# Kernel optimization log

Hardware: AMD Instinct MI355X
Metric: run time of the kernel (lower is better)

## Reference

```python
import jax, jax.numpy as jnp
import numpy as np

B, L, E, H = 512, 100, 256, 256
T = 100          # max_length (== sourceL for TSP)
C_EXPLORE = 10.0  # tanh_exploration
N_GLIMPSES = 1


def setup_inputs() -> dict:
    key = jax.random.key(0)
    ks = jax.random.split(key, 19)
    s = 0.05
    f = lambda k, shape: jax.random.normal(k, shape, dtype=jnp.float32) * s
    return dict(
        decoder_input=f(ks[0], (B, E)),
        embedded_inputs=f(ks[1], (L, B, E)),
        h0=f(ks[2], (B, H)), c0=f(ks[3], (B, H)),
        context=f(ks[4], (L, B, H)),
        Wi=f(ks[5], (4 * H, E)), bi=f(ks[6], (4 * H,)),
        Wh=f(ks[7], (4 * H, H)), bh=f(ks[8], (4 * H,)),
        g_Wq=f(ks[9], (H, H)), g_bq=f(ks[10], (H,)),
        g_Wref=f(ks[11], (H, H)), g_bref=f(ks[12], (H,)),
        g_v=f(ks[13], (H,)),
        p_Wq=f(ks[14], (H, H)), p_bq=f(ks[15], (H,)),
        p_Wref=f(ks[16], (H, H)), p_bref=f(ks[17], (H,)),
        p_v=f(ks[18], (H,)),
    )


def _decode(decoder_input, embedded_inputs, h0, c0, context,
            Wi, bi, Wh, bh,
            g_Wq, g_bq, g_Wref, g_bref, g_v,
            p_Wq, p_bq, p_Wref, p_bref, p_v):
    # Conv1d(dim, dim, 1) over context == feature matmul; context is static,
    # so project refs once (same math as per-step projection in torch code).
    ctx = jnp.transpose(context, (1, 2, 0))                       # [B,H,L]
    e_g = jnp.einsum('oh,bhl->bol', g_Wref, ctx) + g_bref[None, :, None]
    e_p = jnp.einsum('oh,bhl->bol', p_Wref, ctx) + p_bref[None, :, None]
    rows = jnp.arange(B)

    def attn_logits(q, e, Wq, bq, v):
        qp = q @ Wq.T + bq                                        # [B,H]
        return jnp.einsum('h,bhl->bl', v, jnp.tanh(qp[:, :, None] + e))

    def apply_mask(step, logits, mask, prev):
        # step 0: mask position 0; step 1: unmask 0, mask prev; step>1: mask prev
        m1 = jnp.where(step == 1, mask.at[:, 0].set(False), mask)
        m1 = m1.at[rows, prev].set(True)
        m0 = mask.at[:, 0].set(True)
        new_mask = jnp.where(step == 0, m0, m1)
        return jnp.where(new_mask, -jnp.inf, logits), new_mask

    def step_fn(carry, step):
        x, hx, cx, mask, prev = carry
        gates = x @ Wi.T + bi + hx @ Wh.T + bh                    # [B,4H]
        ig, fg, cg, og = jnp.split(gates, 4, axis=1)
        cy = jax.nn.sigmoid(fg) * cx + jax.nn.sigmoid(ig) * jnp.tanh(cg)
        hy = jax.nn.sigmoid(og) * jnp.tanh(cy)
        g_l = hy
        for _ in range(N_GLIMPSES):
            lg = attn_logits(g_l, e_g, g_Wq, g_bq, g_v)
            lg, mask = apply_mask(step, lg, mask, prev)
            g_l = jnp.einsum('bhl,bl->bh', e_g, jax.nn.softmax(lg, axis=1))
        lp = attn_logits(g_l, e_p, p_Wq, p_bq, p_v)
        lp = C_EXPLORE * jnp.tanh(lp)                             # use_tanh=True
        lp, mask = apply_mask(step, lp, mask, prev)
        probs = jax.nn.softmax(lp, axis=1)                        # [B,L]
        idxs = jnp.argmax(probs, axis=1)                          # greedy
        sels = embedded_inputs[idxs, rows, :]                     # [B,E]
        return (sels, hy, cy, mask, idxs), (probs, idxs)

    mask0 = jnp.zeros((B, L), dtype=bool)
    prev0 = jnp.zeros((B,), dtype=jnp.int32)
    carry0 = (decoder_input, h0, c0, mask0, prev0)
    (xT, hx, cx, maskT, prevT), (probs_seq, sel_seq) = jax.lax.scan(
        step_fn, carry0, jnp.arange(T))
    return probs_seq, sel_seq, hx, cx


def reference(decoder_input, embedded_inputs, h0, c0, context,
              Wi, bi, Wh, bh,
              g_Wq, g_bq, g_Wref, g_bref, g_v,
              p_Wq, p_bq, p_Wref, p_bref, p_v):
    return _decode(decoder_input, embedded_inputs, h0, c0, context,
                   Wi, bi, Wh, bh,
                   g_Wq, g_bq, g_Wref, g_bref, g_v,
                   p_Wq, p_bq, p_Wref, p_bref, p_v)
```

## Files before the change

kernel.cpp:

```cpp
#include <hip/hip_runtime.h>
#include <math.h>

namespace {

constexpr int Bn = 512;
constexpr int Ln = 100;
constexpr int En = 256;
constexpr int Hn = 256;
constexpr int Tn = 100;

__device__ __forceinline__ float fast_tanh(float x) {
  float ax = fabsf(x);
  float e = __expf(-2.0f * ax);
  float t = (1.0f - e) / (1.0f + e);
  return copysignf(t, x);
}
__device__ __forceinline__ float fast_sigm(float x) {
  return 1.0f / (1.0f + __expf(-x));
}

__device__ __forceinline__ float wave_max(float v) {
#pragma unroll
  for (int off = 32; off > 0; off >>= 1) v = fmaxf(v, __shfl_xor(v, off, 64));
  return v;
}
__device__ __forceinline__ float wave_sum(float v) {
#pragma unroll
  for (int off = 32; off > 0; off >>= 1) v += __shfl_xor(v, off, 64);
  return v;
}

__global__ void init_kernel(const float* __restrict__ dec, const float* __restrict__ h0,
                            const float* __restrict__ c0, float* __restrict__ x,
                            float* __restrict__ h, float* __restrict__ c,
                            int* __restrict__ mask, int* __restrict__ prev) {
  int i = blockIdx.x * 256 + threadIdx.x;
  if (i < Bn * En) x[i] = dec[i];
  if (i < Bn * Hn) { h[i] = h0[i]; c[i] = c0[i]; }
  if (i < Bn * Ln) mask[i] = 0;
  if (i < Bn) prev[i] = 0;
}

__global__ void transpose256_kernel(const float* __restrict__ W, float* __restrict__ WT) {
  int h = blockIdx.x, k = threadIdx.x;
  WT[k * 256 + h] = W[h * 256 + k];
}

__global__ void matmul_M_kernel(const float* __restrict__ pWq,
                                const float* __restrict__ gWref,
                                float* __restrict__ M) {
  int i = blockIdx.x, j = threadIdx.x;
  float acc = 0.0f;
  for (int h = 0; h < 256; ++h) acc += pWq[i * 256 + h] * gWref[h * 256 + j];
  M[i * 256 + j] = acc;
}

__global__ void mb_kernel(const float* __restrict__ pWq,
                          const float* __restrict__ gbref,
                          float* __restrict__ mb) {
  __shared__ float gb[256];
  int i = threadIdx.x;
  gb[i] = gbref[i];
  __syncthreads();
  float acc = 0.0f;
  for (int h = 0; h < 256; ++h) acc += pWq[i * 256 + h] * gb[h];
  mb[i] = acc;
}

__global__ __launch_bounds__(256) void precompute_e_kernel(
    const float* __restrict__ WT, const float* __restrict__ bref,
    const float* __restrict__ context, float* __restrict__ e_t) {
  int b = blockIdx.x;
  int l0 = blockIdx.y * 25;
  int h = threadIdx.x;
  __shared__ float ctx_s[25][256];
  for (int li = 0; li < 25; ++li)
    ctx_s[li][h] = context[((size_t)(l0 + li) * Bn + b) * Hn + h];
  __syncthreads();
  float acc[25];
  float bias = bref[h];
#pragma unroll
  for (int li = 0; li < 25; ++li) acc[li] = bias;
  for (int k = 0; k < 256; ++k) {
    float w = WT[k * 256 + h];
#pragma unroll
    for (int li = 0; li < 25; ++li) acc[li] += w * ctx_s[li][k];
  }
#pragma unroll
  for (int li = 0; li < 25; ++li)
    e_t[((size_t)b * Ln + (l0 + li)) * Hn + h] = acc[li];
}

__global__ __launch_bounds__(256) void lstm_kernel(
    const float* __restrict__ x, const float* __restrict__ h_in,
    const float* __restrict__ c_in, const float* __restrict__ Wi,
    const float* __restrict__ Wh, const float* __restrict__ bi,
    const float* __restrict__ bh, float* __restrict__ h_out,
    float* __restrict__ c_out) {
  const int b0 = blockIdx.x * 32;
  const int n0 = blockIdx.y * 16;
  const int tid = threadIdx.x;
  const int n = tid & 15;
  const int br = tid >> 4;
  __shared__ float A_s[32][33];
  __shared__ float W_s[4][16][33];
  float acc[4][2];
  const int nn = n0 + n;
#pragma unroll
  for (int g = 0; g < 4; ++g) {
    float bias = bi[g * 256 + nn] + bh[g * 256 + nn];
    acc[g][0] = bias;
    acc[g][1] = bias;
  }
  const int bb = tid >> 3, q = tid & 7;
  for (int k0 = 0; k0 < 512; k0 += 32) {
    const float* Asrc = (k0 < 256) ? x : h_in;
    const float* Wsrc = (k0 < 256) ? Wi : Wh;
    const int kb = k0 & 255;
    __syncthreads();
    float4 av = *(const float4*)(Asrc + (b0 + bb) * 256 + kb + q * 4);
    A_s[q * 4 + 0][bb] = av.x;
    A_s[q * 4 + 1][bb] = av.y;
    A_s[q * 4 + 2][bb] = av.z;
    A_s[q * 4 + 3][bb] = av.w;
#pragma unroll
    for (int s = 0; s < 2; ++s) {
      int sl = tid + s * 256;
      int g = sl >> 7;
      int nl = (sl >> 3) & 15;
      int qq = sl & 7;
      float4 wv = *(const float4*)(Wsrc + ((g * 256 + n0 + nl) * 256) + kb + qq * 4);
      W_s[g][nl][qq * 4 + 0] = wv.x;
      W_s[g][nl][qq * 4 + 1] = wv.y;
      W_s[g][nl][qq * 4 + 2] = wv.z;
      W_s[g][nl][qq * 4 + 3] = wv.w;
    }
    __syncthreads();
#pragma unroll
    for (int kk = 0; kk < 32; ++kk) {
      float a0 = A_s[kk][2 * br];
      float a1 = A_s[kk][2 * br + 1];
#pragma unroll
      for (int g = 0; g < 4; ++g) {
        float w = W_s[g][n][kk];
        acc[g][0] += a0 * w;
        acc[g][1] += a1 * w;
      }
    }
  }
#pragma unroll
  for (int m = 0; m < 2; ++m) {
    int b = b0 + 2 * br + m;
    float ig = acc[0][m], fg = acc[1][m], cg = acc[2][m], og = acc[3][m];
    float cold = c_in[b * 256 + nn];
    float cy = fast_sigm(fg) * cold + fast_sigm(ig) * fast_tanh(cg);
    float hy = fast_sigm(og) * fast_tanh(cy);
    c_out[b * 256 + nn] = cy;
    h_out[b * 256 + nn] = hy;
  }
}

__global__ __launch_bounds__(256) void qp_gemm_kernel(
    const float* __restrict__ A, const float* __restrict__ Wq,
    const float* __restrict__ bq, float* __restrict__ C) {
  const int b0 = blockIdx.x * 32;
  const int n0 = blockIdx.y * 16;
  const int tid = threadIdx.x;
  const int n = tid & 15;
  const int br = tid >> 4;
  __shared__ float A_s[32][33];
  __shared__ float W_s[16][33];
  float bias = bq[n0 + n];
  float acc0 = bias, acc1 = bias;
  const int bb = tid >> 3, q = tid & 7;
  for (int k0 = 0; k0 < 256; k0 += 32) {
    __syncthreads();
    float4 av = *(const float4*)(A + (b0 + bb) * 256 + k0 + q * 4);
    A_s[q * 4 + 0][bb] = av.x;
    A_s[q * 4 + 1][bb] = av.y;
    A_s[q * 4 + 2][bb] = av.z;
    A_s[q * 4 + 3][bb] = av.w;
    if (tid < 128) {
      int nl = tid >> 3, qq = tid & 7;
      float4 wv = *(const float4*)(Wq + (n0 + nl) * 256 + k0 + qq * 4);
      W_s[nl][qq * 4 + 0] = wv.x;
      W_s[nl][qq * 4 + 1] = wv.y;
      W_s[nl][qq * 4 + 2] = wv.z;
      W_s[nl][qq * 4 + 3] = wv.w;
    }
    __syncthreads();
#pragma unroll
    for (int kk = 0; kk < 32; ++kk) {
      float a0 = A_s[kk][2 * br];
      float a1 = A_s[kk][2 * br + 1];
      float w = W_s[n][kk];
      acc0 += a0 * w;
      acc1 += a1 * w;
    }
  }
  C[(b0 + 2 * br) * 256 + n0 + n] = acc0;
  C[(b0 + 2 * br + 1) * 256 + n0 + n] = acc1;
}

__global__ __launch_bounds__(256) void attn_fused_kernel(
    const float* __restrict__ qp_g, const float* __restrict__ gv,
    const float* __restrict__ pv, const float* __restrict__ pbq,
    const float* __restrict__ e_g, const float* __restrict__ f_p,
    const float* __restrict__ e_p, int* __restrict__ mask,
    int* __restrict__ prev, const float* __restrict__ emb,
    float* __restrict__ xout, float* __restrict__ out, int step) {
  const int tid = threadIdx.x;
  const int b = blockIdx.x;
  const int li = tid & 127;
  const int half = tid >> 7;
  __shared__ float q1_s[256], vg_s[256], vp_s[256], q2_s[256];
  __shared__ float logit_s[128], p_s[128];
  __shared__ float wred_m[2], wred_s[2];
  __shared__ float wval[2];
  __shared__ int widx[2];
  __shared__ int sel_s;
  q1_s[tid] = qp_g[b * 256 + tid];
  vg_s[tid] = gv[tid];
  vp_s[tid] = pv[tid];
  __syncthreads();
  float part = 0.0f;
  if (li < Ln) {
    const float4* ep = (const float4*)(e_g + ((size_t)b * Ln + li) * Hn + half * 128);
    const float4* q4 = (const float4*)(q1_s + half * 128);
    const float4* v4 = (const float4*)(vg_s + half * 128);
#pragma unroll 8
    for (int j = 0; j < 32; ++j) {
      float4 ev = ep[j];
      float4 qv = q4[j];
      float4 vv = v4[j];
      part += vv.x * fast_tanh(qv.x + ev.x);
      part += vv.y * fast_tanh(qv.y + ev.y);
      part += vv.z * fast_tanh(qv.z + ev.z);
      part += vv.w * fast_tanh(qv.w + ev.w);
    }
  }
  if (half == 1) logit_s[li] = part;
  __syncthreads();
  float lgv = -INFINITY;
  int mreg = 1;
  if (half == 0 && li < Ln) {
    float a = part + logit_s[li];
    int pb = prev[b];
    int m = mask[b * Ln + li];
    if (step == 0) {
      if (li == 0) m = 1;
    } else {
      if (step == 1 && li == 0) m = 0;
      if (li == pb) m = 1;
    }
    mask[b * Ln + li] = m;
    mreg = m;
    lgv = m ? -INFINITY : a;
  }
  float wm = wave_max((tid < 128) ? lgv : -INFINITY);
  if (tid < 128 && (tid & 63) == 0) wred_m[tid >> 6] = wm;
  __syncthreads();
  float mx = fmaxf(wred_m[0], wred_m[1]);
  float pvv = (lgv == -INFINITY) ? 0.0f : __expf(lgv - mx);
  float wsm = wave_sum((tid < 128) ? pvv : 0.0f);
  if (tid < 128 && (tid & 63) == 0) wred_s[tid >> 6] = wsm;
  __syncthreads();
  float tot = wred_s[0] + wred_s[1];
  if (tid < 128) p_s[li] = pvv / tot;
  __syncthreads();
  {
    float acc = pbq[tid];
    const float* fb = f_p + (size_t)b * Ln * Hn + tid;
#pragma unroll 4
    for (int l = 0; l < Ln; ++l) acc += p_s[l] * fb[(size_t)l * Hn];
    q2_s[tid] = acc;
  }
  __syncthreads();
  part = 0.0f;
  if (li < Ln) {
    const float4* ep = (const float4*)(e_p + ((size_t)b * Ln + li) * Hn + half * 128);
    const float4* q4 = (const float4*)(q2_s + half * 128);
    const float4* v4 = (const float4*)(vp_s + half * 128);
#pragma unroll 8
    for (int j = 0; j < 32; ++j) {
      float4 ev = ep[j];
      float4 qv = q4[j];
      float4 vv = v4[j];
      part += vv.x * fast_tanh(qv.x + ev.x);
      part += vv.y * fast_tanh(qv.y + ev.y);
      part += vv.z * fast_tanh(qv.z + ev.z);
      part += vv.w * fast_tanh(qv.w + ev.w);
    }
  }
  if (half == 1) logit_s[li] = part;
  __syncthreads();
  lgv = -INFINITY;
  if (half == 0 && li < Ln) {
    float a = part + logit_s[li];
    float lp = 10.0f * fast_tanh(a);
    lgv = mreg ? -INFINITY : lp;
  }
  wm = wave_max((tid < 128) ? lgv : -INFINITY);
  if (tid < 128 && (tid & 63) == 0) wred_m[tid >> 6] = wm;
  __syncthreads();
  mx = fmaxf(wred_m[0], wred_m[1]);
  pvv = (lgv == -INFINITY) ? 0.0f : __expf(lgv - mx);
  wsm = wave_sum((tid < 128) ? pvv : 0.0f);
  if (tid < 128 && (tid & 63) == 0) wred_s[tid >> 6] = wsm;
  __syncthreads();
  tot = wred_s[0] + wred_s[1];
  float p = pvv / tot;
  if (half == 0 && li < Ln) out[((size_t)step * Bn + b) * Ln + li] = p;
  float val = (tid < 128 && li < Ln) ? p : -1.0f;
  int idx = li;
#pragma unroll
  for (int off = 32; off > 0; off >>= 1) {
    float ov = __shfl_down(val, off, 64);
    int oi = __shfl_down(idx, off, 64);
    if (ov > val || (ov == val && oi < idx)) { val = ov; idx = oi; }
  }
  if (tid < 128 && (tid & 63) == 0) { wval[tid >> 6] = val; widx[tid >> 6] = idx; }
  __syncthreads();
  if (tid == 0) {
    int sel = (wval[1] > wval[0] || (wval[1] == wval[0] && widx[1] < widx[0]))
                  ? widx[1] : widx[0];
    sel_s = sel;
    prev[b] = sel;
    out[(size_t)Tn * Bn * Ln + (size_t)step * Bn + b] = (float)sel;
  }
  __syncthreads();
  int sel = sel_s;
  xout[b * En + tid] = emb[((size_t)sel * Bn + b) * En + tid];
}

__global__ void finalize_kernel(const float* __restrict__ h,
                                const float* __restrict__ c,
                                float* __restrict__ out) {
  int i = blockIdx.x * 256 + threadIdx.x;
  const size_t base = (size_t)Tn * Bn * Ln + (size_t)Tn * Bn;
  if (i < Bn * Hn) {
    out[base + i] = h[i];
    out[base + (size_t)Bn * Hn + i] = c[i];
  }
}

}

extern "C" void kernel_launch(void* const* d_in, const int* in_sizes, int n_in,
                              void* d_out, int out_size, void* d_ws, size_t ws_size,
                              hipStream_t stream) {
  (void)in_sizes; (void)n_in; (void)out_size; (void)ws_size;
  const float* dec   = (const float*)d_in[0];
  const float* emb   = (const float*)d_in[1];
  const float* h0    = (const float*)d_in[2];
  const float* c0    = (const float*)d_in[3];
  const float* ctx   = (const float*)d_in[4];
  const float* Wi    = (const float*)d_in[5];
  const float* bi    = (const float*)d_in[6];
  const float* Wh    = (const float*)d_in[7];
  const float* bh    = (const float*)d_in[8];
  const float* gWq   = (const float*)d_in[9];
  const float* gbq   = (const float*)d_in[10];
  const float* gWref = (const float*)d_in[11];
  const float* gbref = (const float*)d_in[12];
  const float* gv    = (const float*)d_in[13];
  const float* pWq   = (const float*)d_in[14];
  const float* pbq   = (const float*)d_in[15];
  const float* pWref = (const float*)d_in[16];
  const float* pbref = (const float*)d_in[17];
  const float* pv    = (const float*)d_in[18];

  float* ws = (float*)d_ws;
  float* e_g   = ws;  ws += (size_t)Bn * Hn * Ln;
  float* e_p   = ws;  ws += (size_t)Bn * Hn * Ln;
  float* f_p   = ws;  ws += (size_t)Bn * Hn * Ln;
  float* WTg   = ws;  ws += 256 * 256;
  float* WTp   = ws;  ws += 256 * 256;
  float* Mbuf  = ws;  ws += 256 * 256;
  float* MT    = ws;  ws += 256 * 256;
  float* mb    = ws;  ws += 256;
  float* xbuf  = ws;  ws += Bn * En;
  float* hbuf  = ws;  ws += 2 * Bn * Hn;
  float* cbuf  = ws;  ws += 2 * Bn * Hn;
  float* qpg   = ws;  ws += Bn * Hn;
  int* maskb   = (int*)ws;  ws += Bn * Ln;
  int* prevb   = (int*)ws;  ws += Bn;
  float* out = (float*)d_out;

  init_kernel<<<512, 256, 0, stream>>>(dec, h0, c0, xbuf, hbuf, cbuf, maskb, prevb);
  transpose256_kernel<<<256, 256, 0, stream>>>(gWref, WTg);
  transpose256_kernel<<<256, 256, 0, stream>>>(pWref, WTp);
  matmul_M_kernel<<<256, 256, 0, stream>>>(pWq, gWref, Mbuf);
  mb_kernel<<<1, 256, 0, stream>>>(pWq, gbref, mb);
  transpose256_kernel<<<256, 256, 0, stream>>>(Mbuf, MT);
  precompute_e_kernel<<<dim3(512, 4), 256, 0, stream>>>(WTg, gbref, ctx, e_g);
  precompute_e_kernel<<<dim3(512, 4), 256, 0, stream>>>(WTp, pbref, ctx, e_p);
  precompute_e_kernel<<<dim3(512, 4), 256, 0, stream>>>(MT, mb, ctx, f_p);

  for (int t = 0; t < Tn; ++t) {
    const float* hin = hbuf + (t & 1) * Bn * Hn;
    float* hout      = hbuf + ((t + 1) & 1) * Bn * Hn;
    const float* cin = cbuf + (t & 1) * Bn * Hn;
    float* cout      = cbuf + ((t + 1) & 1) * Bn * Hn;
    lstm_kernel<<<dim3(16, 16), 256, 0, stream>>>(xbuf, hin, cin, Wi, Wh, bi, bh, hout, cout);
    qp_gemm_kernel<<<dim3(16, 16), 256, 0, stream>>>(hout, gWq, gbq, qpg);
    attn_fused_kernel<<<512, 256, 0, stream>>>(qpg, gv, pv, pbq, e_g, f_p, e_p,
                                               maskb, prevb, emb, xbuf, out, t);
  }
  finalize_kernel<<<512, 256, 0, stream>>>(hbuf, cbuf, out);
}
```

Before: 8.001 ms.

## Fuse the per-step decode loop into a single persistent cooperative kernel

Replaces the 300 per-step kernel launches (LSTM GEMM, query GEMM, attention) with one cooperative persistent kernel. It uses grid.sync between the gate GEMM phase and the per-batch attention phase, and computes the glimpse query projection inside each block from a transposed Wq. The goal is to remove launch overhead and intermediate global round-trips. In exchange it adds two grid-wide barriers per step and fixes the grid at 256 blocks, which limits parallelism in the attention phase. It falls back to the old multi-kernel path if the cooperative launch fails.

```diff
diff --git a/kernel.cpp b/kernel.cpp
--- a/kernel.cpp
+++ b/kernel.cpp
@@ -1,5 +1,8 @@
 #include <hip/hip_runtime.h>
+#include <hip/hip_cooperative_groups.h>
 #include <math.h>
+
+namespace cg = cooperative_groups;
 
 namespace {
 
@@ -89,6 +92,248 @@
 #pragma unroll
   for (int li = 0; li < 25; ++li)
     e_t[((size_t)b * Ln + (l0 + li)) * Hn + h] = acc[li];
+}
+
+__global__ __launch_bounds__(256) void persistent_kernel(
+    const float* __restrict__ Wi, const float* __restrict__ Wh,
+    const float* __restrict__ bi, const float* __restrict__ bh,
+    const float* __restrict__ WqTg, const float* __restrict__ gbq,
+    const float* __restrict__ gv, const float* __restrict__ pv,
+    const float* __restrict__ pbq, const float* __restrict__ e_g,
+    const float* __restrict__ f_p, const float* __restrict__ e_p,
+    float* __restrict__ gates, float* __restrict__ xbuf,
+    float* __restrict__ hbuf, float* __restrict__ cbuf,
+    int* __restrict__ mask, int* __restrict__ prev,
+    const float* __restrict__ emb, float* __restrict__ out) {
+  cg::grid_group grid = cg::this_grid();
+  const int blk = blockIdx.x;
+  const int tid = threadIdx.x;
+
+  __shared__ union SM {
+    struct { float A[64][36]; float W[32][36]; } l;
+    struct {
+      float hs[256], q1[256], q2[256], vg[256], vp[256];
+      float qtmp[4][256];
+      float logit[128], p[128];
+      float wred_m[2], wred_s[2], wval[2];
+      int widx[2];
+      int sel;
+    } a;
+  } sm;
+
+  const int nt = blk & 31;
+  const int bt = blk >> 5;
+  const int n0 = nt * 32;
+  const int b0 = bt * 64;
+  const int tx = tid & 15;
+  const int ty = tid >> 4;
+  const int li = tid & 127;
+  const int half = tid >> 7;
+  const size_t hbase = (size_t)Tn * Bn * Ln + (size_t)Tn * Bn;
+  const size_t cbase = hbase + (size_t)Bn * Hn;
+
+  for (int t = 0; t < Tn; ++t) {
+    float acc[4][2];
+    {
+      float bias0 = bi[n0 + 2 * ty] + bh[n0 + 2 * ty];
+      float bias1 = bi[n0 + 2 * ty + 1] + bh[n0 + 2 * ty + 1];
+#pragma unroll
+      for (int i = 0; i < 4; ++i) { acc[i][0] = bias0; acc[i][1] = bias1; }
+    }
+    for (int kc = 0; kc < 16; ++kc) {
+      const float* Asrc = (kc < 8) ? xbuf : hbuf;
+      const float* Wsrc = (kc < 8) ? Wi : Wh;
+      const int kb = (kc & 7) * 32;
+      __syncthreads();
+#pragma unroll
+      for (int i = 0; i < 2; ++i) {
+        int slot = tid + i * 256;
+        int row = slot >> 3, kq = slot & 7;
+        float4 av = *(const float4*)(Asrc + (size_t)(b0 + row) * 256 + kb + kq * 4);
+        *(float4*)&sm.l.A[row][kq * 4] = av;
+      }
+      {
+        int row = tid >> 3, kq = tid & 7;
+        float4 wv = *(const float4*)(Wsrc + (size_t)(n0 + row) * 256 + kb + kq * 4);
+        *(float4*)&sm.l.W[row][kq * 4] = wv;
+      }
+      __syncthreads();
+#pragma unroll
+      for (int kj = 0; kj < 8; ++kj) {
+        float4 aa[4], ww[2];
+#pragma unroll
+        for (int i = 0; i < 4; ++i) aa[i] = *(const float4*)&sm.l.A[4 * tx + i][4 * kj];
+#pragma unroll
+        for (int j = 0; j < 2; ++j) ww[j] = *(const float4*)&sm.l.W[2 * ty + j][4 * kj];
+#pragma unroll
+        for (int i = 0; i < 4; ++i)
+#pragma unroll
+          for (int j = 0; j < 2; ++j)
+            acc[i][j] += aa[i].x * ww[j].x + aa[i].y * ww[j].y +
+                         aa[i].z * ww[j].z + aa[i].w * ww[j].w;
+      }
+    }
+#pragma unroll
+    for (int i = 0; i < 4; ++i) {
+      float2 st = make_float2(acc[i][0], acc[i][1]);
+      *(float2*)&gates[(size_t)(b0 + 4 * tx + i) * 1024 + n0 + 2 * ty] = st;
+    }
+    grid.sync();
+
+    for (int b2 = 0; b2 < 2; ++b2) {
+      const int b = 2 * blk + b2;
+      {
+        float g4[4];
+#pragma unroll
+        for (int g = 0; g < 4; ++g) g4[g] = gates[(size_t)b * 1024 + g * 256 + tid];
+        float cold = cbuf[b * 256 + tid];
+        float cy = fast_sigm(g4[1]) * cold + fast_sigm(g4[0]) * fast_tanh(g4[2]);
+        float hy = fast_sigm(g4[3]) * fast_tanh(cy);
+        cbuf[b * 256 + tid] = cy;
+        hbuf[b * 256 + tid] = hy;
+        sm.a.hs[tid] = hy;
+        if (t == Tn - 1) {
+          out[hbase + b * 256 + tid] = hy;
+          out[cbase + b * 256 + tid] = cy;
+        }
+      }
+      __syncthreads();
+      {
+        int ks = tid >> 6, ho = tid & 63;
+        float ax = 0, ay = 0, az = 0, aw = 0;
+        const float* wb = WqTg + (size_t)ks * 64 * 256 + 4 * ho;
+#pragma unroll 8
+        for (int k = 0; k < 64; ++k) {
+          float hk = sm.a.hs[ks * 64 + k];
+          float4 w = *(const float4*)(wb + (size_t)k * 256);
+          ax += hk * w.x; ay += hk * w.y; az += hk * w.z; aw += hk * w.w;
+        }
+        sm.a.qtmp[ks][4 * ho + 0] = ax;
+        sm.a.qtmp[ks][4 * ho + 1] = ay;
+        sm.a.qtmp[ks][4 * ho + 2] = az;
+        sm.a.qtmp[ks][4 * ho + 3] = aw;
+      }
+      __syncthreads();
+      sm.a.q1[tid] = gbq[tid] + sm.a.qtmp[0][tid] + sm.a.qtmp[1][tid] +
+                     sm.a.qtmp[2][tid] + sm.a.qtmp[3][tid];
+      sm.a.vg[tid] = gv[tid];
+      sm.a.vp[tid] = pv[tid];
+      __syncthreads();
+      float part = 0.0f;
+      if (li < Ln) {
+        const float4* ep = (const float4*)(e_g + ((size_t)b * Ln + li) * Hn + half * 128);
+        const float4* q4 = (const float4*)(sm.a.q1 + half * 128);
+        const float4* v4 = (const float4*)(sm.a.vg + half * 128);
+#pragma unroll 8
+        for (int j = 0; j < 32; ++j) {
+          float4 ev = ep[j];
+          float4 qv = q4[j];
+          float4 vv = v4[j];
+          part += vv.x * fast_tanh(qv.x + ev.x);
+          part += vv.y * fast_tanh(qv.y + ev.y);
+          part += vv.z * fast_tanh(qv.z + ev.z);
+          part += vv.w * fast_tanh(qv.w + ev.w);
+        }
+      }
+      if (half == 1) sm.a.logit[li] = part;
+      __syncthreads();
+      float lgv = -INFINITY;
+      int mreg = 1;
+      if (half == 0 && li < Ln) {
+        float a = part + sm.a.logit[li];
+        int pb = prev[b];
+        int m = mask[b * Ln + li];
+        if (t == 0) {
+          if (li == 0) m = 1;
+        } else {
+          if (t == 1 && li == 0) m = 0;
+          if (li == pb) m = 1;
+        }
+        mask[b * Ln + li] = m;
+        mreg = m;
+        lgv = m ? -INFINITY : a;
+      }
+      float wm = wave_max((tid < 128) ? lgv : -INFINITY);
+      if (tid < 128 && (tid & 63) == 0) sm.a.wred_m[tid >> 6] = wm;
+      __syncthreads();
+      float mx = fmaxf(sm.a.wred_m[0], sm.a.wred_m[1]);
+      float pvv = (lgv == -INFINITY) ? 0.0f : __expf(lgv - mx);
+      float wsm = wave_sum((tid < 128) ? pvv : 0.0f);
+      if (tid < 128 && (tid & 63) == 0) sm.a.wred_s[tid >> 6] = wsm;
+      __syncthreads();
+      float tot = sm.a.wred_s[0] + sm.a.wred_s[1];
+      if (tid < 128) sm.a.p[li] = pvv / tot;
+      __syncthreads();
+      {
+        float accq = pbq[tid];
+        const float* fb = f_p + (size_t)b * Ln * Hn + tid;
+#pragma unroll 4
+        for (int l = 0; l < Ln; ++l) accq += sm.a.p[l] * fb[(size_t)l * Hn];
+        sm.a.q2[tid] = accq;
+      }
+      __syncthreads();
+      part = 0.0f;
+      if (li < Ln) {
+        const float4* ep = (const float4*)(e_p + ((size_t)b * Ln + li) * Hn + half * 128);
+        const float4* q4 = (const float4*)(sm.a.q2 + half * 128);
+        const float4* v4 = (const float4*)(sm.a.vp + half * 128);
+#pragma unroll 8
+        for (int j = 0; j < 32; ++j) {
+          float4 ev = ep[j];
+          float4 qv = q4[j];
+          float4 vv = v4[j];
+          part += vv.x * fast_tanh(qv.x + ev.x);
+          part += vv.y * fast_tanh(qv.y + ev.y);
+          part += vv.z * fast_tanh(qv.z + ev.z);
+          part += vv.w * fast_tanh(qv.w + ev.w);
+        }
+      }
+      if (half == 1) sm.a.logit[li] = part;
+      __syncthreads();
+      lgv = -INFINITY;
+      if (half == 0 && li < Ln) {
+        float a = part + sm.a.logit[li];
+        float lp = 10.0f * fast_tanh(a);
+        lgv = mreg ? -INFINITY : lp;
+      }
+      wm = wave_max((tid < 128) ? lgv : -INFINITY);
+      if (tid < 128 && (tid & 63) == 0) sm.a.wred_m[tid >> 6] = wm;
+      __syncthreads();
+      mx = fmaxf(sm.a.wred_m[0], sm.a.wred_m[1]);
+      pvv = (lgv == -INFINITY) ? 0.0f : __expf(lgv - mx);
+      wsm = wave_sum((tid < 128) ? pvv : 0.0f);
+      if (tid < 128 && (tid & 63) == 0) sm.a.wred_s[tid >> 6] = wsm;
+      __syncthreads();
+      tot = sm.a.wred_s[0] + sm.a.wred_s[1];
+      float p = pvv / tot;
+      if (half == 0 && li < Ln) out[((size_t)t * Bn + b) * Ln + li] = p;
+      float val = (tid < 128 && li < Ln) ? p : -1.0f;
+      int idx = li;
+#pragma unroll
+      for (int off = 32; off > 0; off >>= 1) {
+        float ov = __shfl_down(val, off, 64);
+        int oi = __shfl_down(idx, off, 64);
+        if (ov > val || (ov == val && oi < idx)) { val = ov; idx = oi; }
+      }
+      if (tid < 128 && (tid & 63) == 0) { sm.a.wval[tid >> 6] = val; sm.a.widx[tid >> 6] = idx; }
+      __syncthreads();
+      if (tid == 0) {
+        int sel = (sm.a.wval[1] > sm.a.wval[0] ||
+                   (sm.a.wval[1] == sm.a.wval[0] && sm.a.widx[1] < sm.a.widx[0]))
+                      ? sm.a.widx[1] : sm.a.widx[0];
+        sm.a.sel = sel;
+        prev[b] = sel;
+        out[(size_t)Tn * Bn * Ln + (size_t)t * Bn + b] = (float)sel;
+      }
+      __syncthreads();
+      {
+        int sel = sm.a.sel;
+        xbuf[b * 256 + tid] = emb[((size_t)sel * Bn + b) * En + tid];
+      }
+      __syncthreads();
+    }
+    grid.sync();
+  }
 }
 
 __global__ __launch_bounds__(256) void lstm_kernel(
@@ -378,7 +623,9 @@
   float* WTp   = ws;  ws += 256 * 256;
   float* Mbuf  = ws;  ws += 256 * 256;
   float* MT    = ws;  ws += 256 * 256;
+  float* WqTg  = ws;  ws += 256 * 256;
   float* mb    = ws;  ws += 256;
+  float* gates = ws;  ws += (size_t)Bn * 1024;
   float* xbuf  = ws;  ws += Bn * En;
   float* hbuf  = ws;  ws += 2 * Bn * Hn;
   float* cbuf  = ws;  ws += 2 * Bn * Hn;
@@ -390,6 +637,7 @@
   init_kernel<<<512, 256, 0, stream>>>(dec, h0, c0, xbuf, hbuf, cbuf, maskb, prevb);
   transpose256_kernel<<<256, 256, 0, stream>>>(gWref, WTg);
   transpose256_kernel<<<256, 256, 0, stream>>>(pWref, WTp);
+  transpose256_kernel<<<256, 256, 0, stream>>>(gWq, WqTg);
   matmul_M_kernel<<<256, 256, 0, stream>>>(pWq, gWref, Mbuf);
   mb_kernel<<<1, 256, 0, stream>>>(pWq, gbref, mb);
   transpose256_kernel<<<256, 256, 0, stream>>>(Mbuf, MT);
@@ -397,15 +645,25 @@
   precompute_e_kernel<<<dim3(512, 4), 256, 0, stream>>>(WTp, pbref, ctx, e_p);
   precompute_e_kernel<<<dim3(512, 4), 256, 0, stream>>>(MT, mb, ctx, f_p);
 
-  for (int t = 0; t < Tn; ++t) {
-    const float* hin = hbuf + (t & 1) * Bn * Hn;
-    float* hout      = hbuf + ((t + 1) & 1) * Bn * Hn;
-    const float* cin = cbuf + (t & 1) * Bn * Hn;
-    float* cout      = cbuf + ((t + 1) & 1) * Bn * Hn;
-    lstm_kernel<<<dim3(16, 16), 256, 0, stream>>>(xbuf, hin, cin, Wi, Wh, bi, bh, hout, cout);
-    qp_gemm_kernel<<<dim3(16, 16), 256, 0, stream>>>(hout, gWq, gbq, qpg);
-    attn_fused_kernel<<<512, 256, 0, stream>>>(qpg, gv, pv, pbq, e_g, f_p, e_p,
-                                               maskb, prevb, emb, xbuf, out, t);
-  }
-  finalize_kernel<<<512, 256, 0, stream>>>(hbuf, cbuf, out);
-}
+  void* args[] = {
+      (void*)&Wi, (void*)&Wh, (void*)&bi, (void*)&bh,
+      (void*)&WqTg, (void*)&gbq, (void*)&gv, (void*)&pv,
+      (void*)&pbq, (void*)&e_g, (void*)&f_p, (void*)&e_p,
+      (void*)&gates, (void*)&xbuf, (void*)&hbuf, (void*)&cbuf,
+      (void*)&maskb, (void*)&prevb, (void*)&emb, (void*)&out};
+  hipError_t st = hipLaunchCooperativeKernel((const void*)persistent_kernel,
+                                             dim3(256), dim3(256), args, 0, stream);
+  if (st != hipSuccess) {
+    for (int t = 0; t < Tn; ++t) {
+      const float* hin = hbuf + (t & 1) * Bn * Hn;
+      float* hout      = hbuf + ((t + 1) & 1) * Bn * Hn;
+      const float* cin = cbuf + (t & 1) * Bn * Hn;
+      float* cout      = cbuf + ((t + 1) & 1) * Bn * Hn;
+      lstm_kernel<<<dim3(16, 16), 256, 0, stream>>>(xbuf, hin, cin, Wi, Wh, bi, bh, hout, cout);
+      qp_gemm_kernel<<<dim3(16, 16), 256, 0, stream>>>(hout, gWq, gbq, qpg);
+      attn_fused_kernel<<<512, 256, 0, stream>>>(qpg, gv, pv, pbq, e_g, f_p, e_p,
+                                                 maskb, prevb, emb, xbuf, out, t);
+    }
+    finalize_kernel<<<512, 256, 0, stream>>>(hbuf, cbuf, out);
+  }
+}
```

Result: slower. 19.75 ms (+146.8%).
